# Performance work log

Measured on AMD Instinct MI355X. Metric: run time of the kernel, lower is better.

## Reference

```python
import jax, jax.numpy as jnp
import numpy as np

S, D_MODEL, D_RNN = 256, 512, 512  # module's broadcasting requires d_rnn == d_model


def setup_inputs() -> dict:
    key = jax.random.key(0)
    k1, k2, k3, k4 = jax.random.split(key, 4)
    x = jax.random.normal(k1, (S, D_MODEL), dtype=jnp.float32)
    state = jnp.zeros((D_RNN, D_MODEL), dtype=jnp.float32)
    # equinox nn.Linear default init: U[-1/sqrt(in), 1/sqrt(in)] for weight and bias
    lim = 1.0 / np.sqrt(D_MODEL)
    W1 = jax.random.uniform(k2, (2 * D_RNN, D_MODEL), minval=-lim, maxval=lim, dtype=jnp.float32)
    b1 = jax.random.uniform(k3, (2 * D_RNN,), minval=-lim, maxval=lim, dtype=jnp.float32)
    # Lambda init exactly as in source: inv_sigmoid(p) = log(1/(1-p)), bounds ** (1/8)
    inv_sig = lambda p: np.log(1.0 / (1.0 - p))
    lower = float(np.power(inv_sig(0.9), 1.0 / 8.0))
    upper = float(np.power(inv_sig(0.999), 1.0 / 8.0))
    Lambda = jax.random.uniform(k4, (D_MODEL,), minval=lower, maxval=upper, dtype=jnp.float32)
    return {"x": x, "state": state, "W1": W1, "b1": b1, "Lambda": Lambda}


def reference(x, state, W1, b1, Lambda):
    # lin1 applied per timestep: (S, d_model) @ (d_model, 2*d_rnn)
    z = jax.nn.sigmoid(x @ W1.T + b1)              # (S, 2*d_rnn)
    inp, rec = jnp.split(z, 2, axis=-1)            # each (S, d_rnn)
    # recurrence gate a_t in (0,1): exp(-8 * softplus(Lambda) * rec)
    a = jnp.exp(-8.0 * jax.nn.softplus(Lambda)[None, :] * rec)  # (S, d_rnn)
    # gated input: outer product per step -> (S, d_rnn, d_model)
    gated_x = jnp.einsum('is,is,id->isd', jnp.sqrt(1.0 - a * a), inp, x)

    def step(h, xs):
        g, at = xs
        h = at[:, None] * h + g                    # (d_rnn, d_model)
        return h, h

    state, y = jax.lax.scan(step, state, (gated_x, a))
    return (y, state)
```

## Files before the change

### kernel.cpp

```cpp
#include <hip/hip_runtime.h>
#include <hip/hip_bf16.h>

#define S_LEN 256
#define DM    512
#define DR    512

typedef float f4 __attribute__((ext_vector_type(4)));
typedef float f2 __attribute__((ext_vector_type(2)));

__global__ __launch_bounds__(256) void k_fused(const float* __restrict__ x,
                                               const float* __restrict__ state0,
                                               const float* __restrict__ W1,
                                               const float* __restrict__ b1,
                                               const float* __restrict__ Lam,
                                               f4* __restrict__ out4) {
    const int bx  = blockIdx.x;
    const int sp  = (bx & 7) * 32 + (bx >> 3);
    const int tid = threadIdx.x;
    const int s0  = sp * 2;
    const int s1  = sp * 2 + 1;

    __shared__ f2 ac_l[2][S_LEN];

    {
        const f4* __restrict__ xr  = reinterpret_cast<const f4*>(x) + tid * (DM / 4);
        const f4* __restrict__ wi0 = reinterpret_cast<const f4*>(W1 + s0 * DM);
        const f4* __restrict__ wi1 = reinterpret_cast<const f4*>(W1 + s1 * DM);
        const f4* __restrict__ wr0 = reinterpret_cast<const f4*>(W1 + (DR + s0) * DM);
        const f4* __restrict__ wr1 = reinterpret_cast<const f4*>(W1 + (DR + s1) * DM);

        float ai0 = 0.f, ai1 = 0.f, ar0 = 0.f, ar1 = 0.f;

#pragma unroll 8
        for (int j = 0; j < DM / 4; ++j) {
            const f4 xv = xr[j];
            const f4 a = wi0[j];
            const f4 b = wi1[j];
            const f4 c = wr0[j];
            const f4 d = wr1[j];
            ai0 = fmaf(xv.x, a.x, ai0); ai0 = fmaf(xv.y, a.y, ai0);
            ai0 = fmaf(xv.z, a.z, ai0); ai0 = fmaf(xv.w, a.w, ai0);
            ai1 = fmaf(xv.x, b.x, ai1); ai1 = fmaf(xv.y, b.y, ai1);
            ai1 = fmaf(xv.z, b.z, ai1); ai1 = fmaf(xv.w, b.w, ai1);
            ar0 = fmaf(xv.x, c.x, ar0); ar0 = fmaf(xv.y, c.y, ar0);
            ar0 = fmaf(xv.z, c.z, ar0); ar0 = fmaf(xv.w, c.w, ar0);
            ar1 = fmaf(xv.x, d.x, ar1); ar1 = fmaf(xv.y, d.y, ar1);
            ar1 = fmaf(xv.z, d.z, ar1); ar1 = fmaf(xv.w, d.w, ar1);
        }

#pragma unroll
        for (int j = 0; j < 2; ++j) {
            const float pre_i = (j ? ai1 : ai0) + b1[(j ? s1 : s0)];
            const float pre_r = (j ? ar1 : ar0) + b1[DR + (j ? s1 : s0)];
            const float inp = 1.f / (1.f + expf(-pre_i));
            const float rec = 1.f / (1.f + expf(-pre_r));
            const float sof = log1pf(expf(Lam[(j ? s1 : s0)]));
            const float a   = expf(-8.f * sof * rec);
            const float c   = sqrtf(fmaxf(1.f - a * a, 0.f)) * inp;
            f2 ac; ac.x = a; ac.y = c;
            ac_l[j][tid] = ac;
        }
    }

    const int half = tid >> 7;
    const int s    = sp * 2 + half;
    const int dq   = tid & 127;

    const f4* __restrict__ st4 = reinterpret_cast<const f4*>(state0);
    f4 h = st4[s * 128 + dq];

    const f4* __restrict__ x4 = reinterpret_cast<const f4*>(x);
    f4 xv = x4[dq];

    __syncthreads();

#pragma unroll 4
    for (int t = 0; t < S_LEN; ++t) {
        f4 xn;
        if (t + 1 < S_LEN) xn = x4[(t + 1) * 128 + dq];
        else xn = (f4)0.f;

        const f2 ac = ac_l[half][t];
        const float at = ac.x, ct = ac.y;
        h.x = fmaf(at, h.x, ct * xv.x);
        h.y = fmaf(at, h.y, ct * xv.y);
        h.z = fmaf(at, h.z, ct * xv.z);
        h.w = fmaf(at, h.w, ct * xv.w);

        __builtin_nontemporal_store(h, &out4[(t * DR + s) * 128 + dq]);
        xv = xn;
    }
    out4[(S_LEN * DR) * 128 + s * 128 + dq] = h;
}

extern "C" void kernel_launch(void* const* d_in, const int* in_sizes, int n_in,
                              void* d_out, int out_size, void* d_ws, size_t ws_size,
                              hipStream_t stream) {
    const float* x      = (const float*)d_in[0];
    const float* state0 = (const float*)d_in[1];
    const float* W1     = (const float*)d_in[2];
    const float* b1     = (const float*)d_in[3];
    const float* Lam    = (const float*)d_in[4];

    f4* out4 = (f4*)d_out;

    k_fused<<<dim3(256), 256, 0, stream>>>(x, state0, W1, b1, Lam, out4);
}
```

Before: 69.49 us.

## Restructure gate GEMV prologue to lane-split K with wave shuffle reductions

Replaces the per-thread full-row dot product, where each thread walked its own strided x row, with a layout where each wave covers 64 timesteps. Lanes split the 512-wide reduction dimension, hold their W slices in registers, read x rows coalesced, and combine partial sums with xor-shuffle reductions. Lane 0 writes the gate values to shared memory. This targets uncoalesced global reads in the prologue before the scan, at the cost of many cross-lane shuffles and redundant transcendental evaluation across lanes.

New measurement: 105.1 us. +51.3%, slower.

```diff
diff --git a/kernel.cpp b/kernel.cpp
--- a/kernel.cpp
+++ b/kernel.cpp
@@ -19,46 +19,73 @@
     const int tid = threadIdx.x;
     const int s0  = sp * 2;
     const int s1  = sp * 2 + 1;
+    const int wv  = tid >> 6;
+    const int ln  = tid & 63;
 
     __shared__ f2 ac_l[2][S_LEN];
 
     {
-        const f4* __restrict__ xr  = reinterpret_cast<const f4*>(x) + tid * (DM / 4);
-        const f4* __restrict__ wi0 = reinterpret_cast<const f4*>(W1 + s0 * DM);
-        const f4* __restrict__ wi1 = reinterpret_cast<const f4*>(W1 + s1 * DM);
-        const f4* __restrict__ wr0 = reinterpret_cast<const f4*>(W1 + (DR + s0) * DM);
-        const f4* __restrict__ wr1 = reinterpret_cast<const f4*>(W1 + (DR + s1) * DM);
+        const f4* __restrict__ W4 = reinterpret_cast<const f4*>(W1);
+        const f4* __restrict__ x4 = reinterpret_cast<const f4*>(x);
+        const int kb = ln * 2;
 
-        float ai0 = 0.f, ai1 = 0.f, ar0 = 0.f, ar1 = 0.f;
+        const f4 wi0a = W4[s0 * 128 + kb],        wi0b = W4[s0 * 128 + kb + 1];
+        const f4 wi1a = W4[s1 * 128 + kb],        wi1b = W4[s1 * 128 + kb + 1];
+        const f4 wr0a = W4[(DR + s0) * 128 + kb], wr0b = W4[(DR + s0) * 128 + kb + 1];
+        const f4 wr1a = W4[(DR + s1) * 128 + kb], wr1b = W4[(DR + s1) * 128 + kb + 1];
 
-#pragma unroll 8
-        for (int j = 0; j < DM / 4; ++j) {
-            const f4 xv = xr[j];
-            const f4 a = wi0[j];
-            const f4 b = wi1[j];
-            const f4 c = wr0[j];
-            const f4 d = wr1[j];
-            ai0 = fmaf(xv.x, a.x, ai0); ai0 = fmaf(xv.y, a.y, ai0);
-            ai0 = fmaf(xv.z, a.z, ai0); ai0 = fmaf(xv.w, a.w, ai0);
-            ai1 = fmaf(xv.x, b.x, ai1); ai1 = fmaf(xv.y, b.y, ai1);
-            ai1 = fmaf(xv.z, b.z, ai1); ai1 = fmaf(xv.w, b.w, ai1);
-            ar0 = fmaf(xv.x, c.x, ar0); ar0 = fmaf(xv.y, c.y, ar0);
-            ar0 = fmaf(xv.z, c.z, ar0); ar0 = fmaf(xv.w, c.w, ar0);
-            ar1 = fmaf(xv.x, d.x, ar1); ar1 = fmaf(xv.y, d.y, ar1);
-            ar1 = fmaf(xv.z, d.z, ar1); ar1 = fmaf(xv.w, d.w, ar1);
-        }
+        const float bi0 = b1[s0], bi1 = b1[s1];
+        const float br0 = b1[DR + s0], br1 = b1[DR + s1];
+        const float sof0 = log1pf(expf(Lam[s0]));
+        const float sof1 = log1pf(expf(Lam[s1]));
+
+#pragma unroll 4
+        for (int tt = 0; tt < 64; ++tt) {
+            const int t = wv * 64 + tt;
+            const f4 xa = x4[t * 128 + kb];
+            const f4 xb = x4[t * 128 + kb + 1];
+
+            float p0, p1, p2, p3;
+            p0  = xa.x * wi0a.x; p0 = fmaf(xa.y, wi0a.y, p0);
+            p0  = fmaf(xa.z, wi0a.z, p0); p0 = fmaf(xa.w, wi0a.w, p0);
+            p0  = fmaf(xb.x, wi0b.x, p0); p0 = fmaf(xb.y, wi0b.y, p0);
+            p0  = fmaf(xb.z, wi0b.z, p0); p0 = fmaf(xb.w, wi0b.w, p0);
+            p1  = xa.x * wi1a.x; p1 = fmaf(xa.y, wi1a.y, p1);
+            p1  = fmaf(xa.z, wi1a.z, p1); p1 = fmaf(xa.w, wi1a.w, p1);
+            p1  = fmaf(xb.x, wi1b.x, p1); p1 = fmaf(xb.y, wi1b.y, p1);
+            p1  = fmaf(xb.z, wi1b.z, p1); p1 = fmaf(xb.w, wi1b.w, p1);
+            p2  = xa.x * wr0a.x; p2 = fmaf(xa.y, wr0a.y, p2);
+            p2  = fmaf(xa.z, wr0a.z, p2); p2 = fmaf(xa.w, wr0a.w, p2);
+            p2  = fmaf(xb.x, wr0b.x, p2); p2 = fmaf(xb.y, wr0b.y, p2);
+            p2  = fmaf(xb.z, wr0b.z, p2); p2 = fmaf(xb.w, wr0b.w, p2);
+            p3  = xa.x * wr1a.x; p3 = fmaf(xa.y, wr1a.y, p3);
+            p3  = fmaf(xa.z, wr1a.z, p3); p3 = fmaf(xa.w, wr1a.w, p3);
+            p3  = fmaf(xb.x, wr1b.x, p3); p3 = fmaf(xb.y, wr1b.y, p3);
+            p3  = fmaf(xb.z, wr1b.z, p3); p3 = fmaf(xb.w, wr1b.w, p3);
 
 #pragma unroll
-        for (int j = 0; j < 2; ++j) {
-            const float pre_i = (j ? ai1 : ai0) + b1[(j ? s1 : s0)];
-            const float pre_r = (j ? ar1 : ar0) + b1[DR + (j ? s1 : s0)];
-            const float inp = 1.f / (1.f + expf(-pre_i));
-            const float rec = 1.f / (1.f + expf(-pre_r));
-            const float sof = log1pf(expf(Lam[(j ? s1 : s0)]));
-            const float a   = expf(-8.f * sof * rec);
-            const float c   = sqrtf(fmaxf(1.f - a * a, 0.f)) * inp;
-            f2 ac; ac.x = a; ac.y = c;
-            ac_l[j][tid] = ac;
+            for (int m = 1; m < 64; m <<= 1) {
+                p0 += __shfl_xor(p0, m);
+                p1 += __shfl_xor(p1, m);
+                p2 += __shfl_xor(p2, m);
+                p3 += __shfl_xor(p3, m);
+            }
+
+            const float inp0 = 1.f / (1.f + expf(-(p0 + bi0)));
+            const float inp1 = 1.f / (1.f + expf(-(p1 + bi1)));
+            const float rec0 = 1.f / (1.f + expf(-(p2 + br0)));
+            const float rec1 = 1.f / (1.f + expf(-(p3 + br1)));
+            const float a0 = expf(-8.f * sof0 * rec0);
+            const float a1 = expf(-8.f * sof1 * rec1);
+            const float c0 = sqrtf(fmaxf(1.f - a0 * a0, 0.f)) * inp0;
+            const float c1 = sqrtf(fmaxf(1.f - a1 * a1, 0.f)) * inp1;
+
+            if (ln == 0) {
+                f2 ac0; ac0.x = a0; ac0.y = c0;
+                f2 ac1; ac1.x = a1; ac1.y = c1;
+                ac_l[0][t] = ac0;
+                ac_l[1][t] = ac1;
+            }
         }
     }
 
```
